# Kernel tuning notes

Measured on AMD Instinct MI355X. Metric: run time of the kernel, lower is better.

Reference implementation:

```python
import jax, jax.numpy as jnp
import numpy as np
from jax import lax

# Model constants (from config)
NE, NI = 8192, 2048
N = NE + NI
B, T = 16, 100
K = 512.0
DT = 0.01
TAU_SYN, TAU_NMDA, TAU = 0.02, 0.2, 0.02
DT_SYN, EXP_SYN = DT / TAU_SYN, float(np.exp(-DT / TAU_SYN))
DT_NMDA, EXP_NMDA = DT / TAU_NMDA, float(np.exp(-DT / TAU_NMDA))
DT_TAU, EXP_TAU = DT / TAU, float(np.exp(-DT / TAU))
R_NMDA = 0.4
THRESH = 1.0
USE, TAU_FAC, TAU_REC = 0.03, 1.0, 0.25
GAIN, J_STP = 1.0, 1.0
JAB = np.array([[1.0, -1.5], [1.0, -1.0]], dtype=np.float32)  # E/I block couplings


def setup_inputs() -> dict:
    key = jax.random.key(0)
    k_ff, k_rec, k_mask, k_stp = jax.random.split(key, 4)
    # feedforward drive: positive baseline + noise
    ff_input = 2.0 + 0.5 * jax.random.normal(k_ff, (B, T, N), dtype=jnp.float32)
    rec_input = jax.random.normal(k_rec, (2, B, N), dtype=jnp.float32)
    # sparse E/I connectivity: bernoulli(K/Na_j) mask, J/sqrt(K) weights, transposed (pre x post)
    sizes = [NE, NI]
    offs = [0, NE]
    Wab = np.zeros((N, N), dtype=np.float32)
    rng = np.random.default_rng(0)
    for i in range(2):
        for j in range(2):
            p = K / sizes[j]
            mask = (rng.random((sizes[i], sizes[j])) < p).astype(np.float32)
            Wab[offs[i]:offs[i] + sizes[i], offs[j]:offs[j] + sizes[j]] = JAB[i, j] / np.sqrt(K) * mask
    Wab_T = Wab.T.copy()
    # initSTP: W_stp_T = E->E block / Jab[0,0]; zero E->E block of Wab_T
    W_stp = Wab_T[:NE, :NE] / JAB[0, 0]
    Wab_T[:NE, :NE] = 0.0
    # forward scaling: GAIN * Wab_T, GAIN * J_STP * W_stp_T / sqrt(K)
    Wab_T = GAIN * Wab_T
    W_stp_T = GAIN * J_STP * W_stp / np.sqrt(K)
    return {
        "ff_input": ff_input,
        "rec_input": rec_input,
        "Wab_T": jnp.asarray(Wab_T),
        "W_stp_T": jnp.asarray(W_stp_T),
    }


def _run(ff_input, rec_input, Wab_T, W_stp_T):
    rec0, rec1 = rec_input[0], rec_input[1]
    # initRates: thresholded-relu of ff + rec noise
    rates = jax.nn.relu(ff_input[:, 0] + rec0 - THRESH)
    u0 = jnp.full((B, NE), USE, dtype=jnp.float32)
    x0 = jnp.ones((B, NE), dtype=jnp.float32)
    Wab_E = Wab_T[:NE]  # [NE, N] rows feeding NMDA channel

    def step(carry, ff_t):
        rates, rec0, rec1, u, x = carry
        hidden = rates @ Wab_T                                # [B, N]
        re = rates[:, :NE]
        # STP (Markram) dynamics on E population
        u = u + DT * (USE - u) / TAU_FAC + USE * (1.0 - u) * re * DT
        x = x + DT * (1.0 - x) / TAU_REC - u * x * re * DT
        aux = u * x * re
        h_stp = aux @ W_stp_T                                  # [B, NE]
        hidden = hidden.at[:, :NE].add(h_stp)
        # synaptic leaky integration
        rec0 = rec0 * EXP_SYN + hidden * DT_SYN
        net = ff_t + rec0
        # NMDA channel driven by E rates only
        hidden2 = re @ Wab_E                                   # [B, N]
        hidden2 = hidden2.at[:, :NE].add(h_stp)
        rec1 = rec1 * EXP_NMDA + R_NMDA * hidden2 * DT_NMDA
        net = net + rec1
        # transfer + leaky rate dynamics
        nl = jax.nn.relu(net - THRESH)
        rates = rates * EXP_TAU + nl * DT_TAU
        return (rates, rec0, rec1, u, x), rates

    carry0 = (rates, rec0, rec1, u0, x0)
    _, rates_seq = lax.scan(step, carry0, jnp.swapaxes(ff_input, 0, 1))
    return jnp.swapaxes(rates_seq, 0, 1)  # [B, T, N]


def reference(ff_input, rec_input, Wab_T, W_stp_T):
    return _run(ff_input, rec_input, Wab_T, W_stp_T)
```

## Files before the change

kernel.cpp:

```cpp
#include <hip/hip_runtime.h>
#include <stdint.h>

#define NE 8192
#define NI 2048
#define NN 10240
#define BB 16
#define TT 100
#define NW 320
#define AREC_U32 (640 * 64 * 64)
#define BREC_U32 (640 * 16 * 64)

#define EXP_SYN_C 0.6065306597126334f
#define DT_SYN_C 0.5f
#define EXP_NMDA_C 0.951229424500714f
#define EXP_TAU_C 0.6065306597126334f
#define DT_TAU_C 0.5f
#define USE_C 0.03f
#define SQRTK 22.62741699796952f
#define C_EI (-1.5f / SQRTK)
#define C_IE (1.0f / SQRTK)
#define C_II (-1.0f / SQRTK)
#define C_STP (1.0f / 512.0f)

typedef float floatx4 __attribute__((ext_vector_type(4)));
typedef __bf16 bf16x8 __attribute__((ext_vector_type(8)));

typedef unsigned int u32_g __attribute__((address_space(1)));
typedef unsigned int u32_l __attribute__((address_space(3)));

__device__ __forceinline__ void gld_lds16(const void* g, void* l) {
    __builtin_amdgcn_global_load_lds((const u32_g*)g, (u32_l*)l, 16, 0, 0);
}

__global__ __launch_bounds__(256) void ballot_wab(const float* __restrict__ W,
                                                  uint64_t* __restrict__ bitT) {
    int wv = threadIdx.x >> 6, lane = threadIdx.x & 63;
    int m = blockIdx.x * 4 + wv;
    int c0 = (m < NE) ? 128 : 0;
    const float* row = W + (size_t)m * NN;
    for (int c = c0; c < 160; ++c) {
        uint64_t bits = __ballot(row[c * 64 + lane] != 0.0f);
        if (lane == 0) bitT[(size_t)m * 160 + c] = bits;
    }
}

__global__ __launch_bounds__(256) void ballot_stp(const float* __restrict__ W,
                                                  uint64_t* __restrict__ bitT) {
    int wv = threadIdx.x >> 6, lane = threadIdx.x & 63;
    int m = blockIdx.x * 4 + wv;
    const float* row = W + (size_t)m * NE;
    for (int c = 0; c < 128; ++c) {
        uint64_t bits = __ballot(row[c * 64 + lane] != 0.0f);
        if (lane == 0) bitT[(size_t)m * 160 + c] = bits;
    }
}

__global__ __launch_bounds__(256) void build_rec(const uint32_t* __restrict__ bitT32,
                                                 uint32_t* __restrict__ Arec,
                                                 uint32_t* __restrict__ Brec) {
    int tid = blockIdx.x * 256 + threadIdx.x;
    uint32_t* outp;
    int tau, l, mbase;
    if (tid < AREC_U32) {
        l = tid & 63;
        int g = (tid >> 6) & 63;
        tau = tid >> 12;
        mbase = g * 128;
        outp = Arec + tid;
    } else {
        int t2 = tid - AREC_U32;
        l = t2 & 63;
        int g = (t2 >> 6) & 15;
        tau = t2 >> 10;
        mbase = NE + g * 128;
        outp = Brec + t2;
    }
    int n = tau * 16 + (l & 15);
    int quad = l >> 4;
    int word = n >> 5, bit = n & 31;
    uint32_t out = 0;
    for (int s = 0; s < 4; ++s) {
        int mb = mbase + s * 32 + quad * 8;
        uint32_t byte = 0;
        #pragma unroll
        for (int j = 0; j < 8; ++j) {
            uint32_t w = bitT32[(size_t)(mb + j) * NW + word];
            byte |= ((w >> bit) & 1u) << j;
        }
        out |= byte << (s * 8);
    }
    *outp = out;
}

__device__ __forceinline__ uint32_t bf16rtn(float xf) {
    uint32_t v = __float_as_uint(xf);
    return (v + 0x7FFFu + ((v >> 16) & 1u)) >> 16;
}

__device__ __forceinline__ int fidx(int b, int n) {
    return ((n >> 5) << 9) + ((((n >> 3) & 3) * 16 + b) << 3) + (n & 7);
}

__global__ void init_state(const float* __restrict__ ff, const float* __restrict__ rec_in,
                           float* __restrict__ rates0, float* __restrict__ rec0,
                           float* __restrict__ rec1, float* __restrict__ u,
                           float* __restrict__ x, ushort* __restrict__ Fr0,
                           ushort* __restrict__ Fa0) {
    int tid = blockIdx.x * blockDim.x + threadIdx.x;
    if (tid >= BB * NN) return;
    int b = tid / NN, n = tid - b * NN;
    float r0c = rec_in[tid];
    float r1c = rec_in[BB * NN + tid];
    float f = ff[(size_t)b * TT * NN + n];
    float r = (f + r0c) - 1.0f;
    r = r > 0.0f ? r : 0.0f;
    rates0[tid] = r;
    rec0[tid] = r0c;
    rec1[tid] = r1c;
    Fr0[fidx(b, n)] = (ushort)bf16rtn(r);
    if (n < NE) {
        int o2 = b * NE + n;
        float uu = USE_C;
        uu = uu + 0.01f * (USE_C - uu) + USE_C * (1.0f - uu) * r * 0.01f;
        float xx = 1.0f;
        xx = xx + 0.01f * (1.0f - xx) * 4.0f - uu * xx * r * 0.01f;
        u[o2] = uu;
        x[o2] = xx;
        Fa0[fidx(b, n)] = (ushort)bf16rtn(uu * xx * r);
    }
}

__global__ __launch_bounds__(256) void gemm_step(const ushort* __restrict__ Fr,
                                                 const ushort* __restrict__ Fa,
                                                 const uint32_t* __restrict__ Arec,
                                                 const uint32_t* __restrict__ Brec,
                                                 float* __restrict__ hp) {
    __shared__ ushort bfrag[16384];
    __shared__ uint2 lut[16];
    const int tid = threadIdx.x;
    if (tid < 16) {
        uint32_t p0 = (tid & 1 ? 0x3F80u : 0u) | (tid & 2 ? 0x3F800000u : 0u);
        uint32_t p1 = (tid & 4 ? 0x3F80u : 0u) | (tid & 8 ? 0x3F800000u : 0u);
        lut[tid] = make_uint2(p0, p1);
    }
    const int bid = blockIdx.x;
    int mg, slice, part, recPerTile;
    const uint32_t* rec;
    const ushort* fsrc;
    if (bid < 1280) {
        mg = bid >> 3;
        slice = bid & 7;
        part = slice;
        rec = Arec;
        recPerTile = 64;
        fsrc = (mg < 128 ? Fa : Fr) + slice * (32 * 512);
    } else {
        int b2 = bid - 1280;
        mg = b2 >> 1;
        slice = b2 & 1;
        part = 8 + slice;
        rec = Brec;
        recPerTile = 16;
        fsrc = Fr + (256 + slice * 32) * 512;
    }
    {
        const char* g = (const char*)fsrc + tid * 16;
        char* l = (char*)bfrag + tid * 16;
        #pragma unroll
        for (int i = 0; i < 8; ++i) gld_lds16(g + i * 4096, l + i * 4096);
    }
    const int w = tid >> 6, lane = tid & 63;
    const int tau = mg * 4 + w;
    const uint32_t* recw = rec + (size_t)tau * recPerTile * 64;
    floatx4 acc = {0.f, 0.f, 0.f, 0.f};
    __syncthreads();
    #pragma unroll
    for (int h = 0; h < 8; ++h) {
        uint32_t a32 = recw[(slice * 8 + h) * 64 + lane];
        #pragma unroll
        for (int s = 0; s < 4; ++s) {
            bf16x8 bf = *(const bf16x8*)&bfrag[(h * 4 + s) * 512 + lane * 8];
            uint32_t byte = (a32 >> (s * 8)) & 0xFFu;
            uint2 loE = lut[byte & 15u];
            uint2 hiE = lut[byte >> 4];
            union {
                uint32_t u[4];
                bf16x8 v;
            } af;
            af.u[0] = loE.x;
            af.u[1] = loE.y;
            af.u[2] = hiE.x;
            af.u[3] = hiE.y;
            acc = __builtin_amdgcn_mfma_f32_16x16x32_bf16(af.v, bf, acc, 0, 0, 0);
        }
    }
    float* outp = hp + (size_t)part * (BB * NN);
    int bb = lane & 15, r0 = (lane >> 4) * 4;
    int nb = tau * 16 + r0;
    #pragma unroll
    for (int r = 0; r < 4; ++r) outp[(size_t)bb * NN + nb + r] = acc[r];
}

__global__ __launch_bounds__(256) void update_step(
    const float* __restrict__ ff, int t, const float* __restrict__ hp,
    const float* __restrict__ rates_cur, float* __restrict__ rates_nxt,
    float* __restrict__ u, float* __restrict__ x, ushort* __restrict__ Fr_nxt,
    ushort* __restrict__ Fa_nxt, float* __restrict__ rec0, float* __restrict__ rec1,
    float* __restrict__ out) {
    int tid = blockIdx.x * 256 + threadIdx.x;
    int b = tid / NN, n = tid - b * NN;
    float sA = 0.f, sB = 0.f;
    #pragma unroll
    for (int p = 0; p < 8; ++p) sA += hp[(size_t)p * (BB * NN) + tid];
    sB = hp[(size_t)8 * (BB * NN) + tid] + hp[(size_t)9 * (BB * NN) + tid];
    float hidden, hidden2;
    if (n < NE) {
        float h_stp = C_STP * sA;
        hidden = C_EI * sB + h_stp;
        hidden2 = h_stp;
    } else {
        hidden = C_IE * sA + C_II * sB;
        hidden2 = C_IE * sA;
    }
    float r0 = rec0[tid] * EXP_SYN_C + hidden * DT_SYN_C;
    float r1 = rec1[tid] * EXP_NMDA_C + 0.4f * hidden2 * 0.05f;
    float fv = ff[(size_t)b * TT * NN + (size_t)t * NN + n];
    float net = (fv + r0) + r1;
    float nl = net - 1.0f;
    nl = nl > 0.0f ? nl : 0.0f;
    float rnew = rates_cur[tid] * EXP_TAU_C + nl * DT_TAU_C;
    rec0[tid] = r0;
    rec1[tid] = r1;
    rates_nxt[tid] = rnew;
    out[(size_t)b * TT * NN + (size_t)t * NN + n] = rnew;
    Fr_nxt[fidx(b, n)] = (ushort)bf16rtn(rnew);
    if (n < NE) {
        int o2 = b * NE + n;
        float uu = u[o2];
        uu = uu + 0.01f * (USE_C - uu) + USE_C * (1.0f - uu) * rnew * 0.01f;
        float xx = x[o2];
        xx = xx + 0.01f * (1.0f - xx) * 4.0f - uu * xx * rnew * 0.01f;
        u[o2] = uu;
        x[o2] = xx;
        Fa_nxt[fidx(b, n)] = (ushort)bf16rtn(uu * xx * rnew);
    }
}

extern "C" void kernel_launch(void* const* d_in, const int* in_sizes, int n_in,
                              void* d_out, int out_size, void* d_ws, size_t ws_size,
                              hipStream_t stream) {
    const float* ff = (const float*)d_in[0];
    const float* rec = (const float*)d_in[1];
    const float* Wab_T = (const float*)d_in[2];
    const float* Wstp_T = (const float*)d_in[3];
    float* out = (float*)d_out;

    char* p = (char*)d_ws;
    auto alloc = [&](size_t bytes) {
        char* r = p;
        p += (bytes + 255) & ~(size_t)255;
        return r;
    };
    uint64_t* bitT = (uint64_t*)alloc((size_t)NN * 160 * 8);
    uint32_t* Arec = (uint32_t*)alloc((size_t)AREC_U32 * 4);
    uint32_t* Brec = (uint32_t*)alloc((size_t)BREC_U32 * 4);
    float* hp = (float*)alloc((size_t)10 * BB * NN * 4);
    float* rates0 = (float*)alloc((size_t)NN * BB * 4);
    float* rates1 = (float*)alloc((size_t)NN * BB * 4);
    float* u = (float*)alloc((size_t)NE * BB * 4);
    float* x = (float*)alloc((size_t)NE * BB * 4);
    float* rec0 = (float*)alloc((size_t)NN * BB * 4);
    float* rec1 = (float*)alloc((size_t)NN * BB * 4);
    ushort* Fr0 = (ushort*)alloc((size_t)320 * 512 * 2);
    ushort* Fr1 = (ushort*)alloc((size_t)320 * 512 * 2);
    ushort* Fa0 = (ushort*)alloc((size_t)256 * 512 * 2);
    ushort* Fa1 = (ushort*)alloc((size_t)256 * 512 * 2);

    ballot_wab<<<NN / 4, 256, 0, stream>>>(Wab_T, bitT);
    ballot_stp<<<NE / 4, 256, 0, stream>>>(Wstp_T, bitT);
    build_rec<<<(AREC_U32 + BREC_U32) / 256, 256, 0, stream>>>((const uint32_t*)bitT,
                                                               Arec, Brec);
    init_state<<<(BB * NN + 255) / 256, 256, 0, stream>>>(ff, rec, rates0, rec0, rec1, u,
                                                          x, Fr0, Fa0);
    float* rbuf[2] = {rates0, rates1};
    ushort* Frb[2] = {Fr0, Fr1};
    ushort* Fab[2] = {Fa0, Fa1};
    for (int t = 0; t < TT; ++t) {
        gemm_step<<<1600, 256, 0, stream>>>(Frb[t & 1], Fab[t & 1], Arec, Brec, hp);
        update_step<<<BB * NN / 256, 256, 0, stream>>>(ff, t, hp, rbuf[t & 1],
                                                       rbuf[(t + 1) & 1], u, x,
                                                       Frb[(t + 1) & 1], Fab[(t + 1) & 1],
                                                       rec0, rec1, out);
    }
}
```

Baseline: 2.164 ms.

## Process two output tiles per wave and expand bitmasks arithmetically instead of via LUT

Each wave now computes two 16-column output tiles that share the staged B fragment in LDS, which halves the number of blocks and the redundant LDS staging of the rate fragments. The A bitmask words are all loaded up front, before the barrier, so global latency is exposed earlier. The LDS lookup table for turning bits into bf16 ones is replaced by multiply/mask bit tricks in registers. In exchange it raises register pressure and halves the grid to 800 blocks, which may lower occupancy and latency hiding.

```diff
diff --git a/kernel.cpp b/kernel.cpp
--- a/kernel.cpp
+++ b/kernel.cpp
@@ -130,32 +130,42 @@
     }
 }
 
+__device__ __forceinline__ bf16x8 expand8(uint32_t a32, int s) {
+    uint32_t lo = (a32 >> (8 * s)) & 15u;
+    uint32_t hi = (a32 >> (8 * s + 4)) & 15u;
+    uint32_t sl = (lo * 0x208041u) & 0x01010101u;
+    uint32_t sh = (hi * 0x208041u) & 0x01010101u;
+    union {
+        uint32_t u[4];
+        bf16x8 v;
+    } af;
+    af.u[0] = (sl & 0x10001u) * 0x3F80u;
+    af.u[1] = ((sl >> 8) & 0x10001u) * 0x3F80u;
+    af.u[2] = (sh & 0x10001u) * 0x3F80u;
+    af.u[3] = ((sh >> 8) & 0x10001u) * 0x3F80u;
+    return af.v;
+}
+
 __global__ __launch_bounds__(256) void gemm_step(const ushort* __restrict__ Fr,
                                                  const ushort* __restrict__ Fa,
                                                  const uint32_t* __restrict__ Arec,
                                                  const uint32_t* __restrict__ Brec,
                                                  float* __restrict__ hp) {
     __shared__ ushort bfrag[16384];
-    __shared__ uint2 lut[16];
     const int tid = threadIdx.x;
-    if (tid < 16) {
-        uint32_t p0 = (tid & 1 ? 0x3F80u : 0u) | (tid & 2 ? 0x3F800000u : 0u);
-        uint32_t p1 = (tid & 4 ? 0x3F80u : 0u) | (tid & 8 ? 0x3F800000u : 0u);
-        lut[tid] = make_uint2(p0, p1);
-    }
     const int bid = blockIdx.x;
     int mg, slice, part, recPerTile;
     const uint32_t* rec;
     const ushort* fsrc;
-    if (bid < 1280) {
+    if (bid < 640) {
         mg = bid >> 3;
         slice = bid & 7;
         part = slice;
         rec = Arec;
         recPerTile = 64;
-        fsrc = (mg < 128 ? Fa : Fr) + slice * (32 * 512);
+        fsrc = (mg < 64 ? Fa : Fr) + slice * (32 * 512);
     } else {
-        int b2 = bid - 1280;
+        int b2 = bid - 640;
         mg = b2 >> 1;
         slice = b2 & 1;
         part = 8 + slice;
@@ -170,35 +180,36 @@
         for (int i = 0; i < 8; ++i) gld_lds16(g + i * 4096, l + i * 4096);
     }
     const int w = tid >> 6, lane = tid & 63;
-    const int tau = mg * 4 + w;
-    const uint32_t* recw = rec + (size_t)tau * recPerTile * 64;
-    floatx4 acc = {0.f, 0.f, 0.f, 0.f};
+    const int tau0 = mg * 8 + w * 2;
+    const uint32_t* recw0 = rec + ((size_t)tau0 * recPerTile + slice * 8) * 64 + lane;
+    const uint32_t* recw1 = recw0 + recPerTile * 64;
+    uint32_t a0[8], a1[8];
+    #pragma unroll
+    for (int h = 0; h < 8; ++h) {
+        a0[h] = recw0[h * 64];
+        a1[h] = recw1[h * 64];
+    }
+    floatx4 acc0 = {0.f, 0.f, 0.f, 0.f};
+    floatx4 acc1 = {0.f, 0.f, 0.f, 0.f};
     __syncthreads();
     #pragma unroll
     for (int h = 0; h < 8; ++h) {
-        uint32_t a32 = recw[(slice * 8 + h) * 64 + lane];
         #pragma unroll
         for (int s = 0; s < 4; ++s) {
             bf16x8 bf = *(const bf16x8*)&bfrag[(h * 4 + s) * 512 + lane * 8];
-            uint32_t byte = (a32 >> (s * 8)) & 0xFFu;
-            uint2 loE = lut[byte & 15u];
-            uint2 hiE = lut[byte >> 4];
-            union {
-                uint32_t u[4];
-                bf16x8 v;
-            } af;
-            af.u[0] = loE.x;
-            af.u[1] = loE.y;
-            af.u[2] = hiE.x;
-            af.u[3] = hiE.y;
-            acc = __builtin_amdgcn_mfma_f32_16x16x32_bf16(af.v, bf, acc, 0, 0, 0);
+            acc0 = __builtin_amdgcn_mfma_f32_16x16x32_bf16(expand8(a0[h], s), bf, acc0,
+                                                           0, 0, 0);
+            acc1 = __builtin_amdgcn_mfma_f32_16x16x32_bf16(expand8(a1[h], s), bf, acc1,
+                                                           0, 0, 0);
         }
     }
     float* outp = hp + (size_t)part * (BB * NN);
     int bb = lane & 15, r0 = (lane >> 4) * 4;
-    int nb = tau * 16 + r0;
-    #pragma unroll
-    for (int r = 0; r < 4; ++r) outp[(size_t)bb * NN + nb + r] = acc[r];
+    int nb0 = tau0 * 16 + r0;
+    #pragma unroll
+    for (int r = 0; r < 4; ++r) outp[(size_t)bb * NN + nb0 + r] = acc0[r];
+    #pragma unroll
+    for (int r = 0; r < 4; ++r) outp[(size_t)bb * NN + nb0 + 16 + r] = acc1[r];
 }
 
 __global__ __launch_bounds__(256) void update_step(
@@ -286,7 +297,7 @@
     ushort* Frb[2] = {Fr0, Fr1};
     ushort* Fab[2] = {Fa0, Fa1};
     for (int t = 0; t < TT; ++t) {
-        gemm_step<<<1600, 256, 0, stream>>>(Frb[t & 1], Fab[t & 1], Arec, Brec, hp);
+        gemm_step<<<800, 256, 0, stream>>>(Frb[t & 1], Fab[t & 1], Arec, Brec, hp);
         update_step<<<BB * NN / 256, 256, 0, stream>>>(ff, t, hp, rbuf[t & 1],
                                                        rbuf[(t + 1) & 1], u, x,
                                                        Frb[(t + 1) & 1], Fab[(t + 1) & 1],
```

Result: slower. 2.457 ms (+13.6%).

## Compute four output tiles per wave to reuse B fragments across tiles

Applied to the files above, without the earlier changes.

Each wave in the bit-packed GEMM now computes four 16-column output tiles over a shorter K slice instead of one tile over a longer slice. Each LDS B fragment is reused across four MFMAs, and all A records are loaded up front. The split-K count doubles (20 partial buffers instead of 10), so the update kernel reads twice as many partial sums. Block count halves to 800, and per-block LDS is halved.

```diff
diff --git a/kernel.cpp b/kernel.cpp
--- a/kernel.cpp
+++ b/kernel.cpp
@@ -135,7 +135,7 @@
                                                  const uint32_t* __restrict__ Arec,
                                                  const uint32_t* __restrict__ Brec,
                                                  float* __restrict__ hp) {
-    __shared__ ushort bfrag[16384];
+    __shared__ ushort bfrag[8192];
     __shared__ uint2 lut[16];
     const int tid = threadIdx.x;
     if (tid < 16) {
@@ -144,43 +144,52 @@
         lut[tid] = make_uint2(p0, p1);
     }
     const int bid = blockIdx.x;
-    int mg, slice, part, recPerTile;
+    int tg, sl, part, gpt;
     const uint32_t* rec;
     const ushort* fsrc;
-    if (bid < 1280) {
-        mg = bid >> 3;
-        slice = bid & 7;
-        part = slice;
+    if (bid < 640) {
+        tg = bid >> 4;
+        sl = bid & 15;
+        part = sl;
         rec = Arec;
-        recPerTile = 64;
-        fsrc = (mg < 128 ? Fa : Fr) + slice * (32 * 512);
+        gpt = 64;
+        fsrc = (tg < 32 ? Fa : Fr) + sl * (16 * 512);
     } else {
-        int b2 = bid - 1280;
-        mg = b2 >> 1;
-        slice = b2 & 1;
-        part = 8 + slice;
+        int b2 = bid - 640;
+        tg = b2 >> 2;
+        sl = b2 & 3;
+        part = 16 + sl;
         rec = Brec;
-        recPerTile = 16;
-        fsrc = Fr + (256 + slice * 32) * 512;
+        gpt = 16;
+        fsrc = Fr + (256 + sl * 16) * 512;
     }
     {
         const char* g = (const char*)fsrc + tid * 16;
         char* l = (char*)bfrag + tid * 16;
         #pragma unroll
-        for (int i = 0; i < 8; ++i) gld_lds16(g + i * 4096, l + i * 4096);
+        for (int i = 0; i < 4; ++i) gld_lds16(g + i * 4096, l + i * 4096);
     }
     const int w = tid >> 6, lane = tid & 63;
-    const int tau = mg * 4 + w;
-    const uint32_t* recw = rec + (size_t)tau * recPerTile * 64;
-    floatx4 acc = {0.f, 0.f, 0.f, 0.f};
+    const int tau0 = tg * 16 + w * 4;
+    const int g0 = sl * 4;
+    uint32_t a[4][4];
+    #pragma unroll
+    for (int ta = 0; ta < 4; ++ta) {
+        const uint32_t* rp = rec + ((size_t)(tau0 + ta) * gpt + g0) * 64 + lane;
+        #pragma unroll
+        for (int gg = 0; gg < 4; ++gg) a[ta][gg] = rp[gg * 64];
+    }
+    floatx4 acc[4];
+    #pragma unroll
+    for (int ta = 0; ta < 4; ++ta) acc[ta] = (floatx4){0.f, 0.f, 0.f, 0.f};
     __syncthreads();
     #pragma unroll
-    for (int h = 0; h < 8; ++h) {
-        uint32_t a32 = recw[(slice * 8 + h) * 64 + lane];
-        #pragma unroll
-        for (int s = 0; s < 4; ++s) {
-            bf16x8 bf = *(const bf16x8*)&bfrag[(h * 4 + s) * 512 + lane * 8];
-            uint32_t byte = (a32 >> (s * 8)) & 0xFFu;
+    for (int ks = 0; ks < 16; ++ks) {
+        bf16x8 bf = *(const bf16x8*)&bfrag[ks * 512 + lane * 8];
+        const int gg = ks >> 2, s = ks & 3;
+        #pragma unroll
+        for (int ta = 0; ta < 4; ++ta) {
+            uint32_t byte = (a[ta][gg] >> (s * 8)) & 0xFFu;
             uint2 loE = lut[byte & 15u];
             uint2 hiE = lut[byte >> 4];
             union {
@@ -191,14 +200,17 @@
             af.u[1] = loE.y;
             af.u[2] = hiE.x;
             af.u[3] = hiE.y;
-            acc = __builtin_amdgcn_mfma_f32_16x16x32_bf16(af.v, bf, acc, 0, 0, 0);
+            acc[ta] = __builtin_amdgcn_mfma_f32_16x16x32_bf16(af.v, bf, acc[ta], 0, 0, 0);
         }
     }
     float* outp = hp + (size_t)part * (BB * NN);
     int bb = lane & 15, r0 = (lane >> 4) * 4;
-    int nb = tau * 16 + r0;
-    #pragma unroll
-    for (int r = 0; r < 4; ++r) outp[(size_t)bb * NN + nb + r] = acc[r];
+    #pragma unroll
+    for (int ta = 0; ta < 4; ++ta) {
+        int nb = (tau0 + ta) * 16 + r0;
+        #pragma unroll
+        for (int r = 0; r < 4; ++r) outp[(size_t)bb * NN + nb + r] = acc[ta][r];
+    }
 }
 
 __global__ __launch_bounds__(256) void update_step(
@@ -211,8 +223,9 @@
     int b = tid / NN, n = tid - b * NN;
     float sA = 0.f, sB = 0.f;
     #pragma unroll
-    for (int p = 0; p < 8; ++p) sA += hp[(size_t)p * (BB * NN) + tid];
-    sB = hp[(size_t)8 * (BB * NN) + tid] + hp[(size_t)9 * (BB * NN) + tid];
+    for (int p = 0; p < 16; ++p) sA += hp[(size_t)p * (BB * NN) + tid];
+    #pragma unroll
+    for (int p = 16; p < 20; ++p) sB += hp[(size_t)p * (BB * NN) + tid];
     float hidden, hidden2;
     if (n < NE) {
         float h_stp = C_STP * sA;
@@ -264,7 +277,7 @@
     uint64_t* bitT = (uint64_t*)alloc((size_t)NN * 160 * 8);
     uint32_t* Arec = (uint32_t*)alloc((size_t)AREC_U32 * 4);
     uint32_t* Brec = (uint32_t*)alloc((size_t)BREC_U32 * 4);
-    float* hp = (float*)alloc((size_t)10 * BB * NN * 4);
+    float* hp = (float*)alloc((size_t)20 * BB * NN * 4);
     float* rates0 = (float*)alloc((size_t)NN * BB * 4);
     float* rates1 = (float*)alloc((size_t)NN * BB * 4);
     float* u = (float*)alloc((size_t)NE * BB * 4);
@@ -286,7 +299,7 @@
     ushort* Frb[2] = {Fr0, Fr1};
     ushort* Fab[2] = {Fa0, Fa1};
     for (int t = 0; t < TT; ++t) {
-        gemm_step<<<1600, 256, 0, stream>>>(Frb[t & 1], Fab[t & 1], Arec, Brec, hp);
+        gemm_step<<<800, 256, 0, stream>>>(Frb[t & 1], Fab[t & 1], Arec, Brec, hp);
         update_step<<<BB * NN / 256, 256, 0, stream>>>(ff, t, hp, rbuf[t & 1],
                                                        rbuf[(t + 1) & 1], u, x,
                                                        Frb[(t + 1) & 1], Fab[(t + 1) & 1],
```

Result: slower. 2.475 ms (+14.4%).

## Fuse GEMM and state update via per-column-group arrival counter, last-block-finishes

Applied to the files above, without the earlier changes.

Merges the per-timestep GEMM and elementwise update kernels into one launch. Each block stores its partial sums with agent-scope atomics and increments a per-column-group counter, and the last of the 10 contributing blocks reduces the partials and performs the rate, STP and synaptic updates with vectorized accesses. The rec-matrix loads are also hoisted ahead of the LDS barrier. This removes 100 kernel launches and the global round-trip gap between them, at the cost of atomic counter traffic and the update work being serialized onto the late-finishing blocks.

```diff
diff --git a/kernel.cpp b/kernel.cpp
--- a/kernel.cpp
+++ b/kernel.cpp
@@ -105,8 +105,9 @@
                            float* __restrict__ rates0, float* __restrict__ rec0,
                            float* __restrict__ rec1, float* __restrict__ u,
                            float* __restrict__ x, ushort* __restrict__ Fr0,
-                           ushort* __restrict__ Fa0) {
+                           ushort* __restrict__ Fa0, int* __restrict__ cnt) {
     int tid = blockIdx.x * blockDim.x + threadIdx.x;
+    if (tid < 160) cnt[tid] = 0;
     if (tid >= BB * NN) return;
     int b = tid / NN, n = tid - b * NN;
     float r0c = rec_in[tid];
@@ -130,13 +131,17 @@
     }
 }
 
-__global__ __launch_bounds__(256) void gemm_step(const ushort* __restrict__ Fr,
-                                                 const ushort* __restrict__ Fa,
-                                                 const uint32_t* __restrict__ Arec,
-                                                 const uint32_t* __restrict__ Brec,
-                                                 float* __restrict__ hp) {
+__global__ __launch_bounds__(256) void fused_step(
+    const float* __restrict__ ff, int t, const ushort* __restrict__ Fr,
+    const ushort* __restrict__ Fa, const uint32_t* __restrict__ Arec,
+    const uint32_t* __restrict__ Brec, float* __restrict__ hp, int* __restrict__ cnt,
+    const float* __restrict__ rates_cur, float* __restrict__ rates_nxt,
+    float* __restrict__ u, float* __restrict__ x, ushort* __restrict__ Fr_nxt,
+    ushort* __restrict__ Fa_nxt, float* __restrict__ rec0, float* __restrict__ rec1,
+    float* __restrict__ out) {
     __shared__ ushort bfrag[16384];
     __shared__ uint2 lut[16];
+    __shared__ int winner_s;
     const int tid = threadIdx.x;
     if (tid < 16) {
         uint32_t p0 = (tid & 1 ? 0x3F80u : 0u) | (tid & 2 ? 0x3F800000u : 0u);
@@ -145,13 +150,13 @@
     }
     const int bid = blockIdx.x;
     int mg, slice, part, recPerTile;
-    const uint32_t* rec;
+    const uint32_t* recp;
     const ushort* fsrc;
     if (bid < 1280) {
         mg = bid >> 3;
         slice = bid & 7;
         part = slice;
-        rec = Arec;
+        recp = Arec;
         recPerTile = 64;
         fsrc = (mg < 128 ? Fa : Fr) + slice * (32 * 512);
     } else {
@@ -159,7 +164,7 @@
         mg = b2 >> 1;
         slice = b2 & 1;
         part = 8 + slice;
-        rec = Brec;
+        recp = Brec;
         recPerTile = 16;
         fsrc = Fr + (256 + slice * 32) * 512;
     }
@@ -171,16 +176,18 @@
     }
     const int w = tid >> 6, lane = tid & 63;
     const int tau = mg * 4 + w;
-    const uint32_t* recw = rec + (size_t)tau * recPerTile * 64;
+    const uint32_t* recw = recp + ((size_t)tau * recPerTile + slice * 8) * 64 + lane;
+    uint32_t a[8];
+    #pragma unroll
+    for (int h = 0; h < 8; ++h) a[h] = recw[h * 64];
     floatx4 acc = {0.f, 0.f, 0.f, 0.f};
     __syncthreads();
     #pragma unroll
     for (int h = 0; h < 8; ++h) {
-        uint32_t a32 = recw[(slice * 8 + h) * 64 + lane];
         #pragma unroll
         for (int s = 0; s < 4; ++s) {
             bf16x8 bf = *(const bf16x8*)&bfrag[(h * 4 + s) * 512 + lane * 8];
-            uint32_t byte = (a32 >> (s * 8)) & 0xFFu;
+            uint32_t byte = (a[h] >> (s * 8)) & 0xFFu;
             uint2 loE = lut[byte & 15u];
             uint2 hiE = lut[byte >> 4];
             union {
@@ -194,55 +201,91 @@
             acc = __builtin_amdgcn_mfma_f32_16x16x32_bf16(af.v, bf, acc, 0, 0, 0);
         }
     }
-    float* outp = hp + (size_t)part * (BB * NN);
-    int bb = lane & 15, r0 = (lane >> 4) * 4;
-    int nb = tau * 16 + r0;
+    {
+        float* outp = hp + (size_t)part * (BB * NN) + (size_t)(lane & 15) * NN +
+                      tau * 16 + (lane >> 4) * 4;
+        #pragma unroll
+        for (int r = 0; r < 4; ++r)
+            __hip_atomic_store(&outp[r], acc[r], __ATOMIC_RELAXED,
+                               __HIP_MEMORY_SCOPE_AGENT);
+    }
+    __syncthreads();
+    if (tid == 0) {
+        int old = __hip_atomic_fetch_add(&cnt[mg], 1, __ATOMIC_ACQ_REL,
+                                         __HIP_MEMORY_SCOPE_AGENT);
+        winner_s = (old == t * 10 + 9) ? 1 : 0;
+    }
+    __syncthreads();
+    if (!winner_s) return;
+    const int b = tid >> 4;
+    const int n0 = mg * 64 + (tid & 15) * 4;
+    const int e0 = b * NN + n0;
+    float sA[4] = {0.f, 0.f, 0.f, 0.f}, sB[4] = {0.f, 0.f, 0.f, 0.f};
     #pragma unroll
-    for (int r = 0; r < 4; ++r) outp[(size_t)bb * NN + nb + r] = acc[r];
-}
-
-__global__ __launch_bounds__(256) void update_step(
-    const float* __restrict__ ff, int t, const float* __restrict__ hp,
-    const float* __restrict__ rates_cur, float* __restrict__ rates_nxt,
-    float* __restrict__ u, float* __restrict__ x, ushort* __restrict__ Fr_nxt,
-    ushort* __restrict__ Fa_nxt, float* __restrict__ rec0, float* __restrict__ rec1,
-    float* __restrict__ out) {
-    int tid = blockIdx.x * 256 + threadIdx.x;
-    int b = tid / NN, n = tid - b * NN;
-    float sA = 0.f, sB = 0.f;
+    for (int pp = 0; pp < 10; ++pp) {
+        #pragma unroll
+        for (int k = 0; k < 4; ++k) {
+            float v = __hip_atomic_load(hp + (size_t)pp * (BB * NN) + e0 + k,
+                                        __ATOMIC_RELAXED, __HIP_MEMORY_SCOPE_AGENT);
+            if (pp < 8) sA[k] += v;
+            else sB[k] += v;
+        }
+    }
+    const bool isE = (n0 < NE);
+    floatx4 r0v = *(const floatx4*)(rec0 + e0);
+    floatx4 r1v = *(const floatx4*)(rec1 + e0);
+    floatx4 rcv = *(const floatx4*)(rates_cur + e0);
+    floatx4 fv = *(const floatx4*)(ff + (size_t)b * TT * NN + (size_t)t * NN + n0);
+    floatx4 rnv, auxv;
     #pragma unroll
-    for (int p = 0; p < 8; ++p) sA += hp[(size_t)p * (BB * NN) + tid];
-    sB = hp[(size_t)8 * (BB * NN) + tid] + hp[(size_t)9 * (BB * NN) + tid];
-    float hidden, hidden2;
-    if (n < NE) {
-        float h_stp = C_STP * sA;
-        hidden = C_EI * sB + h_stp;
-        hidden2 = h_stp;
-    } else {
-        hidden = C_IE * sA + C_II * sB;
-        hidden2 = C_IE * sA;
-    }
-    float r0 = rec0[tid] * EXP_SYN_C + hidden * DT_SYN_C;
-    float r1 = rec1[tid] * EXP_NMDA_C + 0.4f * hidden2 * 0.05f;
-    float fv = ff[(size_t)b * TT * NN + (size_t)t * NN + n];
-    float net = (fv + r0) + r1;
-    float nl = net - 1.0f;
-    nl = nl > 0.0f ? nl : 0.0f;
-    float rnew = rates_cur[tid] * EXP_TAU_C + nl * DT_TAU_C;
-    rec0[tid] = r0;
-    rec1[tid] = r1;
-    rates_nxt[tid] = rnew;
-    out[(size_t)b * TT * NN + (size_t)t * NN + n] = rnew;
-    Fr_nxt[fidx(b, n)] = (ushort)bf16rtn(rnew);
-    if (n < NE) {
-        int o2 = b * NE + n;
-        float uu = u[o2];
-        uu = uu + 0.01f * (USE_C - uu) + USE_C * (1.0f - uu) * rnew * 0.01f;
-        float xx = x[o2];
-        xx = xx + 0.01f * (1.0f - xx) * 4.0f - uu * xx * rnew * 0.01f;
-        u[o2] = uu;
-        x[o2] = xx;
-        Fa_nxt[fidx(b, n)] = (ushort)bf16rtn(uu * xx * rnew);
+    for (int k = 0; k < 4; ++k) {
+        float hidden, hidden2;
+        if (isE) {
+            float h_stp = C_STP * sA[k];
+            hidden = C_EI * sB[k] + h_stp;
+            hidden2 = h_stp;
+        } else {
+            hidden = C_IE * sA[k] + C_II * sB[k];
+            hidden2 = C_IE * sA[k];
+        }
+        float r0 = r0v[k] * EXP_SYN_C + hidden * DT_SYN_C;
+        float r1 = r1v[k] * EXP_NMDA_C + 0.4f * hidden2 * 0.05f;
+        float net = (fv[k] + r0) + r1;
+        float nl = net - 1.0f;
+        nl = nl > 0.0f ? nl : 0.0f;
+        float rnew = rcv[k] * EXP_TAU_C + nl * DT_TAU_C;
+        r0v[k] = r0;
+        r1v[k] = r1;
+        rnv[k] = rnew;
+    }
+    *(floatx4*)(rec0 + e0) = r0v;
+    *(floatx4*)(rec1 + e0) = r1v;
+    *(floatx4*)(rates_nxt + e0) = rnv;
+    *(floatx4*)(out + (size_t)b * TT * NN + (size_t)t * NN + n0) = rnv;
+    {
+        uint32_t w01 = bf16rtn(rnv[0]) | (bf16rtn(rnv[1]) << 16);
+        uint32_t w23 = bf16rtn(rnv[2]) | (bf16rtn(rnv[3]) << 16);
+        *(uint2*)(Fr_nxt + fidx(b, n0)) = make_uint2(w01, w23);
+    }
+    if (isE) {
+        int o2 = b * NE + n0;
+        floatx4 uv = *(const floatx4*)(u + o2);
+        floatx4 xv = *(const floatx4*)(x + o2);
+        #pragma unroll
+        for (int k = 0; k < 4; ++k) {
+            float uu = uv[k];
+            uu = uu + 0.01f * (USE_C - uu) + USE_C * (1.0f - uu) * rnv[k] * 0.01f;
+            float xx = xv[k];
+            xx = xx + 0.01f * (1.0f - xx) * 4.0f - uu * xx * rnv[k] * 0.01f;
+            uv[k] = uu;
+            xv[k] = xx;
+            auxv[k] = uu * xx * rnv[k];
+        }
+        *(floatx4*)(u + o2) = uv;
+        *(floatx4*)(x + o2) = xv;
+        uint32_t w01 = bf16rtn(auxv[0]) | (bf16rtn(auxv[1]) << 16);
+        uint32_t w23 = bf16rtn(auxv[2]) | (bf16rtn(auxv[3]) << 16);
+        *(uint2*)(Fa_nxt + fidx(b, n0)) = make_uint2(w01, w23);
     }
 }
 
@@ -275,21 +318,21 @@
     ushort* Fr1 = (ushort*)alloc((size_t)320 * 512 * 2);
     ushort* Fa0 = (ushort*)alloc((size_t)256 * 512 * 2);
     ushort* Fa1 = (ushort*)alloc((size_t)256 * 512 * 2);
+    int* cnt = (int*)alloc(160 * 4);
 
     ballot_wab<<<NN / 4, 256, 0, stream>>>(Wab_T, bitT);
     ballot_stp<<<NE / 4, 256, 0, stream>>>(Wstp_T, bitT);
     build_rec<<<(AREC_U32 + BREC_U32) / 256, 256, 0, stream>>>((const uint32_t*)bitT,
                                                                Arec, Brec);
     init_state<<<(BB * NN + 255) / 256, 256, 0, stream>>>(ff, rec, rates0, rec0, rec1, u,
-                                                          x, Fr0, Fa0);
+                                                          x, Fr0, Fa0, cnt);
     float* rbuf[2] = {rates0, rates1};
     ushort* Frb[2] = {Fr0, Fr1};
     ushort* Fab[2] = {Fa0, Fa1};
     for (int t = 0; t < TT; ++t) {
-        gemm_step<<<1600, 256, 0, stream>>>(Frb[t & 1], Fab[t & 1], Arec, Brec, hp);
-        update_step<<<BB * NN / 256, 256, 0, stream>>>(ff, t, hp, rbuf[t & 1],
-                                                       rbuf[(t + 1) & 1], u, x,
-                                                       Frb[(t + 1) & 1], Fab[(t + 1) & 1],
-                                                       rec0, rec1, out);
-    }
-}
+        fused_step<<<1600, 256, 0, stream>>>(ff, t, Frb[t & 1], Fab[t & 1], Arec, Brec,
+                                             hp, cnt, rbuf[t & 1], rbuf[(t + 1) & 1], u,
+                                             x, Frb[(t + 1) & 1], Fab[(t + 1) & 1], rec0,
+                                             rec1, out);
+    }
+}
```

Measured after the change: 5.185 ms. 140% more time.
